# Kernel optimization log

Hardware: AMD Instinct MI355X
Metric: run time of the kernel (lower is better)

## Reference

```python
import jax, jax.numpy as jnp
import numpy as np

N = 50000
E = 800000
IN_DIM = 128
H1 = 512
H2 = 300
OUT_DIM = 10
EPS = 1e-5


def setup_inputs() -> dict:
    key = jax.random.key(0)
    ks = jax.random.split(key, 12)
    x = jax.random.normal(ks[0], (N, IN_DIM), dtype=jnp.float32)
    edge_index = jax.random.randint(ks[1], (2, E), 0, N, dtype=jnp.int64)
    edge_weight = jax.random.uniform(ks[2], (E,), dtype=jnp.float32)
    def glorot(k, fan_in, fan_out):
        lim = np.sqrt(6.0 / (fan_in + fan_out)).astype(np.float32)
        return jax.random.uniform(k, (fan_in, fan_out), jnp.float32, -lim, lim)
    return {
        "x": x,
        "edge_index": edge_index,
        "edge_weight": edge_weight,
        "W1": glorot(ks[3], IN_DIM, H1), "b1": jnp.zeros((H1,), jnp.float32),
        "g1": jnp.ones((H1,), jnp.float32), "beta1": jnp.zeros((H1,), jnp.float32),
        "W2": glorot(ks[4], H1, H2), "b2": jnp.zeros((H2,), jnp.float32),
        "g2": jnp.ones((H2,), jnp.float32), "beta2": jnp.zeros((H2,), jnp.float32),
        "Wl": glorot(ks[5], H2, OUT_DIM), "bl": jnp.zeros((OUT_DIM,), jnp.float32),
    }


def _gcn_norm(edge_index, edge_weight, n):
    # add self loops (fill value 1.0), then symmetric normalization (PyG gcn_norm)
    si = jnp.arange(n, dtype=edge_index.dtype)
    row = jnp.concatenate([edge_index[0], si])  # source
    col = jnp.concatenate([edge_index[1], si])  # target
    w = jnp.concatenate([edge_weight, jnp.ones((n,), edge_weight.dtype)])
    deg = jax.ops.segment_sum(w, col, num_segments=n)
    dis = jnp.where(deg > 0, jax.lax.rsqrt(deg), 0.0)
    return row, col, dis[row] * w * dis[col]


def _propagate(h, row, col, norm, n):
    # gather source rows, weight, scatter-add into targets
    return jax.ops.segment_sum(h[row] * norm[:, None], col, num_segments=n)


def _batchnorm(h, g, beta):
    mean = jnp.mean(h, axis=0)
    var = jnp.mean(jnp.square(h - mean), axis=0)  # biased var (torch BN)
    return (h - mean) * jax.lax.rsqrt(var + EPS) * g + beta


def reference(x, edge_index, edge_weight, W1, b1, g1, beta1,
              W2, b2, g2, beta2, Wl, bl):
    n = x.shape[0]
    row, col, norm = _gcn_norm(edge_index, edge_weight, n)
    # layer 1: aggregate then transform (== GCNConv's lin-then-propagate math)
    h = _propagate(x, row, col, norm, n) @ W1 + b1
    h = jax.nn.relu(_batchnorm(h, g1, beta1))
    # layer 2: transform then aggregate
    h = _propagate(h @ W2, row, col, norm, n) + b2
    h = jax.nn.relu(_batchnorm(h, g2, beta2))
    # classifier head + log_softmax
    h = jax.nn.relu(h @ Wl + bl)
    return jax.nn.log_softmax(h, axis=1)
```

## Files before the change

kernel.cpp:

```cpp
#include <hip/hip_runtime.h>
#include <math.h>

namespace {

constexpr int kIn  = 128;
constexpr int kH1  = 512;
constexpr int kH2  = 300;
constexpr int kH2p = 304;
constexpr int kOut = 10;
constexpr float kEps = 1e-5f;

typedef __attribute__((ext_vector_type(8))) short bf16x8;
typedef __attribute__((ext_vector_type(4))) float f32x4;

__device__ __forceinline__ void atomAddF(float* p, float v) {
  unsafeAtomicAdd(p, v);
}

__device__ __forceinline__ unsigned short f2bf(float f) {
  unsigned u = __builtin_bit_cast(unsigned, f);
  unsigned r = u + 0x7fffu + ((u >> 16) & 1u);
  return (unsigned short)(r >> 16);
}

__device__ __forceinline__ float bf2f(unsigned short h) {
  return __builtin_bit_cast(float, (unsigned)h << 16);
}

__device__ __forceinline__ float blo(unsigned u) {
  return __builtin_bit_cast(float, u << 16);
}
__device__ __forceinline__ float bhi(unsigned u) {
  return __builtin_bit_cast(float, u & 0xffff0000u);
}

__device__ __forceinline__ void fma8(const uint4& q, float w, float* acc) {
  acc[0] = fmaf(blo(q.x), w, acc[0]);
  acc[1] = fmaf(bhi(q.x), w, acc[1]);
  acc[2] = fmaf(blo(q.y), w, acc[2]);
  acc[3] = fmaf(bhi(q.y), w, acc[3]);
  acc[4] = fmaf(blo(q.z), w, acc[4]);
  acc[5] = fmaf(bhi(q.z), w, acc[5]);
  acc[6] = fmaf(blo(q.w), w, acc[6]);
  acc[7] = fmaf(bhi(q.w), w, acc[7]);
}

__global__ void k_init(float* __restrict__ deg, int* __restrict__ cnt, int n) {
  int i = blockIdx.x * blockDim.x + threadIdx.x;
  if (i < n) { deg[i] = 1.0f; cnt[i] = 0; }
}

__global__ void k_deg_cnt(float* __restrict__ deg, int* __restrict__ cnt,
                          const int* __restrict__ ei, const float* __restrict__ w, int nE) {
  int i = blockIdx.x * blockDim.x + threadIdx.x;
  if (i < nE) {
    int c = ei[nE + i];
    atomAddF(&deg[c], w[i]);
    atomicAdd(&cnt[c], 1);
  }
}

__global__ void k_dis(float* __restrict__ deg, int n) {
  int i = blockIdx.x * blockDim.x + threadIdx.x;
  if (i < n) deg[i] = rsqrtf(deg[i]);
}

__global__ __launch_bounds__(1024) void k_scan(int* __restrict__ cnt, int n) {
  __shared__ int wsum[16];
  __shared__ int woff[17];
  const int lane = threadIdx.x & 63;
  const int wid  = threadIdx.x >> 6;
  int carry = 0;
  const int nchunk = (n + 1023) >> 10;
  for (int ch = 0; ch < nchunk; ++ch) {
    int i = (ch << 10) + threadIdx.x;
    int v = (i < n) ? cnt[i] : 0;
    int s = v;
#pragma unroll
    for (int off = 1; off < 64; off <<= 1) {
      int t = __shfl_up(s, off);
      if (lane >= off) s += t;
    }
    if (lane == 63) wsum[wid] = s;
    __syncthreads();
    if (wid == 0 && lane < 16) {
      int u = wsum[lane];
#pragma unroll
      for (int off = 1; off < 16; off <<= 1) {
        int q = __shfl_up(u, off);
        if (lane >= off) u += q;
      }
      woff[lane + 1] = u;
      if (lane == 0) woff[0] = 0;
    }
    __syncthreads();
    int excl = s - v + woff[wid] + carry;
    if (i < n) cnt[i] = excl;
    carry += woff[16];
    __syncthreads();
  }
}

__global__ void k_scatter(int* __restrict__ cnt, const int* __restrict__ ei,
                          const float* __restrict__ w, const float* __restrict__ dis,
                          uint2* __restrict__ pr, int nE) {
  int i = blockIdx.x * blockDim.x + threadIdx.x;
  if (i < nE) {
    int r = ei[i];
    int c = ei[nE + i];
    int pos = atomicAdd(&cnt[c], 1);
    float ww = dis[r] * w[i] * dis[c];
    pr[pos] = make_uint2((unsigned)r, __builtin_bit_cast(unsigned, ww));
  }
}

__global__ void k_xbf(const float* __restrict__ X, unsigned short* __restrict__ O, int total4) {
  int i = blockIdx.x * blockDim.x + threadIdx.x;
  if (i >= total4) return;
  float4 v = reinterpret_cast<const float4*>(X)[i];
  uint2 pk;
  pk.x = (unsigned)f2bf(v.x) | ((unsigned)f2bf(v.y) << 16);
  pk.y = (unsigned)f2bf(v.z) | ((unsigned)f2bf(v.w) << 16);
  reinterpret_cast<uint2*>(O)[i] = pk;
}

__global__ void k_wt(const float* __restrict__ W, unsigned short* __restrict__ WT,
                     int K, int Nsrc, int Npad) {
  int idx = blockIdx.x * blockDim.x + threadIdx.x;
  if (idx >= K * Npad) return;
  int n = idx / K, k = idx - n * K;
  WT[idx] = (n < Nsrc) ? f2bf(W[(size_t)k * Nsrc + n]) : (unsigned short)0;
}

template<int NSQ>
__global__ void k_gather(const unsigned short* __restrict__ X, const int* __restrict__ endp,
                         const uint2* __restrict__ pr, const float* __restrict__ dis,
                         unsigned short* __restrict__ out, int n) {
  int tid = blockIdx.x * blockDim.x + threadIdx.x;
  int v = tid / NSQ;
  int s = tid - v * NSQ;
  if (v >= n) return;
  int beg = (v == 0) ? 0 : endp[v - 1];
  int end = endp[v];
  const uint4* Xr = reinterpret_cast<const uint4*>(X);
  float d = dis[v];
  float sw = d * d;
  float acc[8];
  {
    uint4 q = Xr[(size_t)v * NSQ + s];
    acc[0] = blo(q.x) * sw; acc[1] = bhi(q.x) * sw;
    acc[2] = blo(q.y) * sw; acc[3] = bhi(q.y) * sw;
    acc[4] = blo(q.z) * sw; acc[5] = bhi(q.z) * sw;
    acc[6] = blo(q.w) * sw; acc[7] = bhi(q.w) * sw;
  }
  int e = beg;
  for (; e + 4 <= end; e += 4) {
    uint2 p0 = pr[e], p1 = pr[e + 1], p2 = pr[e + 2], p3 = pr[e + 3];
    uint4 q0 = Xr[(size_t)p0.x * NSQ + s];
    uint4 q1 = Xr[(size_t)p1.x * NSQ + s];
    uint4 q2 = Xr[(size_t)p2.x * NSQ + s];
    uint4 q3 = Xr[(size_t)p3.x * NSQ + s];
    fma8(q0, __builtin_bit_cast(float, p0.y), acc);
    fma8(q1, __builtin_bit_cast(float, p1.y), acc);
    fma8(q2, __builtin_bit_cast(float, p2.y), acc);
    fma8(q3, __builtin_bit_cast(float, p3.y), acc);
  }
  for (; e < end; ++e) {
    uint2 p = pr[e];
    uint4 q = Xr[(size_t)p.x * NSQ + s];
    fma8(q, __builtin_bit_cast(float, p.y), acc);
  }
  uint4 o;
  o.x = (unsigned)f2bf(acc[0]) | ((unsigned)f2bf(acc[1]) << 16);
  o.y = (unsigned)f2bf(acc[2]) | ((unsigned)f2bf(acc[3]) << 16);
  o.z = (unsigned)f2bf(acc[4]) | ((unsigned)f2bf(acc[5]) << 16);
  o.w = (unsigned)f2bf(acc[6]) | ((unsigned)f2bf(acc[7]) << 16);
  reinterpret_cast<uint4*>(out)[(size_t)v * NSQ + s] = o;
}

__global__ __launch_bounds__(256) void k_gemm(const unsigned short* __restrict__ A,
                                              const unsigned short* __restrict__ BT,
                                              unsigned short* __restrict__ C, int M, int Nlog, int K) {
  constexpr int BM = 128, BN = 128, BK = 32;
  __shared__ unsigned short lA[(BK / 8) * BM * 8];
  __shared__ unsigned short lB[(BK / 8) * BN * 8];
  const int tid  = threadIdx.x;
  const int lane = tid & 63;
  const int wid  = tid >> 6;
  const int wr   = wid >> 1;
  const int wc   = wid & 1;
  const int m0 = blockIdx.x * BM;
  const int n0 = blockIdx.y * BN;

  const int sm  = tid >> 2;
  const int sk8 = tid & 3;
  const int fr = lane & 15, fq = lane >> 4;

  f32x4 acc[4][4] = {};

  for (int k0 = 0; k0 < K; k0 += BK) {
    uint4 a0, a1, b0, b1;
    {
      const uint4 z = make_uint4(0, 0, 0, 0);
      int r0 = m0 + sm, r1 = m0 + sm + 64;
      a0 = (r0 < M) ? *reinterpret_cast<const uint4*>(A + (size_t)r0 * K + k0 + sk8 * 8) : z;
      a1 = (r1 < M) ? *reinterpret_cast<const uint4*>(A + (size_t)r1 * K + k0 + sk8 * 8) : z;
      int c0 = n0 + sm, c1 = n0 + sm + 64;
      b0 = (c0 < Nlog) ? *reinterpret_cast<const uint4*>(BT + (size_t)c0 * K + k0 + sk8 * 8) : z;
      b1 = (c1 < Nlog) ? *reinterpret_cast<const uint4*>(BT + (size_t)c1 * K + k0 + sk8 * 8) : z;
    }
    __syncthreads();
    *reinterpret_cast<uint4*>(lA + (sk8 * BM + sm) * 8)      = a0;
    *reinterpret_cast<uint4*>(lA + (sk8 * BM + sm + 64) * 8) = a1;
    *reinterpret_cast<uint4*>(lB + (sk8 * BN + sm) * 8)      = b0;
    *reinterpret_cast<uint4*>(lB + (sk8 * BN + sm + 64) * 8) = b1;
    __syncthreads();

    bf16x8 af[4], bfr[4];
#pragma unroll
    for (int m = 0; m < 4; ++m)
      af[m] = *reinterpret_cast<const bf16x8*>(lA + (fq * BM + wr * 64 + m * 16 + fr) * 8);
#pragma unroll
    for (int nn = 0; nn < 4; ++nn)
      bfr[nn] = *reinterpret_cast<const bf16x8*>(lB + (fq * BN + wc * 64 + nn * 16 + fr) * 8);
#pragma unroll
    for (int m = 0; m < 4; ++m)
#pragma unroll
      for (int nn = 0; nn < 4; ++nn)
        acc[m][nn] = __builtin_amdgcn_mfma_f32_16x16x32_bf16(af[m], bfr[nn], acc[m][nn], 0, 0, 0);
  }

#pragma unroll
  for (int m = 0; m < 4; ++m) {
#pragma unroll
    for (int r = 0; r < 4; ++r) {
      int row = m0 + wr * 64 + m * 16 + fq * 4 + r;
      if (row >= M) continue;
#pragma unroll
      for (int nn = 0; nn < 4; ++nn) {
        int col = n0 + wc * 64 + nn * 16 + fr;
        if (col < Nlog)
          C[(size_t)row * Nlog + col] = f2bf(acc[m][nn][r]);
      }
    }
  }
}

__global__ void k_bn_stats_bf16(const unsigned short* __restrict__ H, float* __restrict__ s1,
                                float* __restrict__ s2, int n, int C, int stride, int rpb) {
  int r0 = blockIdx.x * rpb;
  int r1 = r0 + rpb;
  if (r1 > n) r1 = n;
  for (int c = threadIdx.x; c < C; c += blockDim.x) {
    float a = 0.f, b = 0.f;
    for (int r = r0; r < r1; ++r) {
      float v = bf2f(H[(size_t)r * stride + c]);
      a += v;
      b = fmaf(v, v, b);
    }
    atomAddF(&s1[c], a);
    atomAddF(&s2[c], b);
  }
}

__global__ void k_bn_finalize(const float* __restrict__ s1, const float* __restrict__ s2,
                              const float* __restrict__ g, const float* __restrict__ beta,
                              float* __restrict__ scale, float* __restrict__ shift,
                              int C, float invN) {
  int c = blockIdx.x * blockDim.x + threadIdx.x;
  if (c >= C) return;
  float mean = s1[c] * invN;
  float var = fmaxf(s2[c] * invN - mean * mean, 0.f);
  float sc = g[c] * rsqrtf(var + kEps);
  scale[c] = sc;
  shift[c] = beta[c] - mean * sc;
}

template<int C>
__global__ void k_bn_apply_relu_bf16(unsigned short* __restrict__ H,
                                     const float* __restrict__ scale,
                                     const float* __restrict__ shift, int total8) {
  int i = blockIdx.x * blockDim.x + threadIdx.x;
  if (i >= total8) return;
  uint4 q = reinterpret_cast<uint4*>(H)[i];
  int c = (i * 8) & (C - 1);
  unsigned w[4] = {q.x, q.y, q.z, q.w};
  unsigned o[4];
#pragma unroll
  for (int j = 0; j < 4; ++j) {
    float lo = blo(w[j]);
    float hi = bhi(w[j]);
    int cl = c + j * 2;
    lo = fmaxf(fmaf(lo, scale[cl],     shift[cl]),     0.f);
    hi = fmaxf(fmaf(hi, scale[cl + 1], shift[cl + 1]), 0.f);
    o[j] = (unsigned)f2bf(lo) | ((unsigned)f2bf(hi) << 16);
  }
  reinterpret_cast<uint4*>(H)[i] = make_uint4(o[0], o[1], o[2], o[3]);
}

__global__ __launch_bounds__(256) void k_head(const unsigned short* __restrict__ H,
    const float* __restrict__ scale, const float* __restrict__ shift,
    const float* __restrict__ Wl, const float* __restrict__ bl,
    float* __restrict__ out, int n) {
  __shared__ float sW[kH2 * kOut];
  __shared__ float sScale[kH2], sShift[kH2];
  for (int i = threadIdx.x; i < kH2 * kOut; i += blockDim.x) sW[i] = Wl[i];
  for (int i = threadIdx.x; i < kH2; i += blockDim.x) {
    sScale[i] = scale[i];
    sShift[i] = shift[i];
  }
  __syncthreads();
  float blv[kOut];
#pragma unroll
  for (int j = 0; j < kOut; ++j) blv[j] = bl[j];
  const int lane = threadIdx.x & 63;
  const int wid = (blockIdx.x * blockDim.x + threadIdx.x) >> 6;
  const int nw  = (gridDim.x * blockDim.x) >> 6;
  for (int node = wid; node < n; node += nw) {
    const unsigned short* hrow = H + (size_t)node * kH2p;
    float acc[kOut] = {};
    for (int k = lane; k < kH2; k += 64) {
      float v = fmaxf(fmaf(bf2f(hrow[k]), sScale[k], sShift[k]), 0.f);
      const float* wr = sW + k * kOut;
#pragma unroll
      for (int j = 0; j < kOut; ++j) acc[j] = fmaf(v, wr[j], acc[j]);
    }
#pragma unroll
    for (int j = 0; j < kOut; ++j) {
      float v = acc[j];
      for (int off = 32; off > 0; off >>= 1) v += __shfl_down(v, off);
      acc[j] = v;
    }
    if (lane == 0) {
      float vv[kOut], m = -1e30f;
#pragma unroll
      for (int j = 0; j < kOut; ++j) {
        vv[j] = fmaxf(acc[j] + blv[j], 0.f);
        m = fmaxf(m, vv[j]);
      }
      float s = 0.f;
#pragma unroll
      for (int j = 0; j < kOut; ++j) s += expf(vv[j] - m);
      float lse = m + logf(s);
      float* o = out + (size_t)node * kOut;
#pragma unroll
      for (int j = 0; j < kOut; ++j) o[j] = vv[j] - lse;
    }
  }
}

}

extern "C" void kernel_launch(void* const* d_in, const int* in_sizes, int n_in,
                              void* d_out, int out_size, void* d_ws, size_t ws_size,
                              hipStream_t stream) {
  const float* x   = (const float*)d_in[0];
  const int*   ei  = (const int*)d_in[1];
  const float* ew  = (const float*)d_in[2];
  const float* W1  = (const float*)d_in[3];
  const float* g1  = (const float*)d_in[5];
  const float* be1 = (const float*)d_in[6];
  const float* W2  = (const float*)d_in[7];
  const float* g2  = (const float*)d_in[9];
  const float* be2 = (const float*)d_in[10];
  const float* Wl  = (const float*)d_in[11];
  const float* bl  = (const float*)d_in[12];
  float* out = (float*)d_out;
  float* ws  = (float*)d_ws;

  const int n = in_sizes[0] / kIn;
  const int e = in_sizes[1] / 2;

  float* dis = ws;
  int*   cnt = (int*)(ws + 50048);
  uint2* pr  = (uint2*)(ws + 100096);
  float* st  = ws + 1700096;
  float* s1a = st,        *s2a = st + 512,  *sc1 = st + 1024, *sh1 = st + 1536;
  float* s1b = st + 2048, *s2b = st + 2560, *sc2 = st + 3072, *sh2 = st + 3584;
  unsigned short* xbf = (unsigned short*)(ws + 1704192);
  unsigned short* W1T = (unsigned short*)(ws + 4904192);
  unsigned short* W2T = (unsigned short*)(ws + 4936960);
  unsigned short* slotA = (unsigned short*)(ws + 5014784);
  unsigned short* slotB = (unsigned short*)(ws + 12614784);
  unsigned short* agg1 = slotA;
  unsigned short* t2   = slotA;
  unsigned short* h1   = slotB;
  unsigned short* agg2 = slotB;

  constexpr int TPB = 256;

  k_init<<<(n + TPB - 1) / TPB, TPB, 0, stream>>>(dis, cnt, n);
  k_deg_cnt<<<(e + TPB - 1) / TPB, TPB, 0, stream>>>(dis, cnt, ei, ew, e);
  k_dis<<<(n + TPB - 1) / TPB, TPB, 0, stream>>>(dis, n);
  k_scan<<<1, 1024, 0, stream>>>(cnt, n);
  k_scatter<<<(e + TPB - 1) / TPB, TPB, 0, stream>>>(cnt, ei, ew, dis, pr, e);
  hipMemsetAsync(st, 0, 4096 * sizeof(float), stream);
  k_xbf<<<(n * (kIn / 4) + TPB - 1) / TPB, TPB, 0, stream>>>(x, xbf, n * (kIn / 4));
  k_wt<<<(kIn * kH1 + TPB - 1) / TPB, TPB, 0, stream>>>(W1, W1T, kIn, kH1, kH1);
  k_wt<<<(kH1 * kH2p + TPB - 1) / TPB, TPB, 0, stream>>>(W2, W2T, kH1, kH2, kH2p);

  {
    int tot = n * (kIn / 8);
    k_gather<kIn / 8><<<(tot + TPB - 1) / TPB, TPB, 0, stream>>>(xbf, cnt, pr, dis, agg1, n);
  }
  {
    dim3 g((n + 127) / 128, kH1 / 128);
    k_gemm<<<g, 256, 0, stream>>>(agg1, W1T, h1, n, kH1, kIn);
  }
  k_bn_stats_bf16<<<512, 256, 0, stream>>>(h1, s1a, s2a, n, kH1, kH1, (n + 511) / 512);
  k_bn_finalize<<<(kH1 + 255) / 256, 256, 0, stream>>>(s1a, s2a, g1, be1, sc1, sh1, kH1, 1.0f / n);
  k_bn_apply_relu_bf16<kH1><<<((n * (kH1 / 8)) + TPB - 1) / TPB, TPB, 0, stream>>>(
      h1, sc1, sh1, n * (kH1 / 8));

  {
    dim3 g((n + 127) / 128, (kH2p + 127) / 128);
    k_gemm<<<g, 256, 0, stream>>>(h1, W2T, t2, n, kH2p, kH1);
  }
  {
    int tot = n * (kH2p / 8);
    k_gather<kH2p / 8><<<(tot + TPB - 1) / TPB, TPB, 0, stream>>>(t2, cnt, pr, dis, agg2, n);
  }
  k_bn_stats_bf16<<<512, 256, 0, stream>>>(agg2, s1b, s2b, n, kH2, kH2p, (n + 511) / 512);
  k_bn_finalize<<<(kH2 + 255) / 256, 256, 0, stream>>>(s1b, s2b, g2, be2, sc2, sh2, kH2, 1.0f / n);

  k_head<<<1024, 256, 0, stream>>>(agg2, sc2, sh2, Wl, bl, out, n);
}
```

Baseline: 562.2 us.

## Slice gather features by column for cache locality, fuse BN into GEMM, merge prep kernels

The gather inputs are stored in column-slice-major layout: 8 slices of 16 columns for x, and 8 slices of 40 columns for t2 after padding H2 to 320. Each gather block then works on one slice, so the random row reads touch a smaller working set that fits better in L2. Layer-1 BN+ReLU is applied while loading the A operand of the second GEMM, which drops a separate read-modify-write pass over h1. Conversion, weight transpose and zero-init are merged into a single prep kernel. In exchange the padding adds GEMM and gather work, the edge lists are re-read once per slice, and the workspace needs more separate buffers.

```diff
diff --git a/kernel.cpp b/kernel.cpp
--- a/kernel.cpp
+++ b/kernel.cpp
@@ -6,32 +6,27 @@
 constexpr int kIn  = 128;
 constexpr int kH1  = 512;
 constexpr int kH2  = 300;
-constexpr int kH2p = 304;
+constexpr int kH2p = 320;
 constexpr int kOut = 10;
 constexpr float kEps = 1e-5f;
 
 typedef __attribute__((ext_vector_type(8))) short bf16x8;
 typedef __attribute__((ext_vector_type(4))) float f32x4;
 
-__device__ __forceinline__ void atomAddF(float* p, float v) {
-  unsafeAtomicAdd(p, v);
-}
+__device__ __forceinline__ void atomAddF(float* p, float v) { unsafeAtomicAdd(p, v); }
 
 __device__ __forceinline__ unsigned short f2bf(float f) {
   unsigned u = __builtin_bit_cast(unsigned, f);
   unsigned r = u + 0x7fffu + ((u >> 16) & 1u);
   return (unsigned short)(r >> 16);
 }
-
 __device__ __forceinline__ float bf2f(unsigned short h) {
   return __builtin_bit_cast(float, (unsigned)h << 16);
 }
-
-__device__ __forceinline__ float blo(unsigned u) {
-  return __builtin_bit_cast(float, u << 16);
-}
-__device__ __forceinline__ float bhi(unsigned u) {
-  return __builtin_bit_cast(float, u & 0xffff0000u);
+__device__ __forceinline__ float blo(unsigned u) { return __builtin_bit_cast(float, u << 16); }
+__device__ __forceinline__ float bhi(unsigned u) { return __builtin_bit_cast(float, u & 0xffff0000u); }
+__device__ __forceinline__ unsigned pk2(float a, float b) {
+  return (unsigned)f2bf(a) | ((unsigned)f2bf(b) << 16);
 }
 
 __device__ __forceinline__ void fma8(const uint4& q, float w, float* acc) {
@@ -45,9 +40,41 @@
   acc[7] = fmaf(bhi(q.w), w, acc[7]);
 }
 
-__global__ void k_init(float* __restrict__ deg, int* __restrict__ cnt, int n) {
+__device__ __forceinline__ uint4 bnpack(uint4 q, float4 s0, float4 s1, float4 h0, float4 h1) {
+  uint4 r;
+  r.x = pk2(fmaxf(fmaf(blo(q.x), s0.x, h0.x), 0.f), fmaxf(fmaf(bhi(q.x), s0.y, h0.y), 0.f));
+  r.y = pk2(fmaxf(fmaf(blo(q.y), s0.z, h0.z), 0.f), fmaxf(fmaf(bhi(q.y), s0.w, h0.w), 0.f));
+  r.z = pk2(fmaxf(fmaf(blo(q.z), s1.x, h1.x), 0.f), fmaxf(fmaf(bhi(q.z), s1.y, h1.y), 0.f));
+  r.w = pk2(fmaxf(fmaf(blo(q.w), s1.z, h1.z), 0.f), fmaxf(fmaf(bhi(q.w), s1.w, h1.w), 0.f));
+  return r;
+}
+
+__global__ void k_prep(float* __restrict__ deg, int* __restrict__ cnt,
+                       const float* __restrict__ x, unsigned short* __restrict__ xbf,
+                       float* __restrict__ st,
+                       const float* __restrict__ W1, unsigned short* __restrict__ W1T,
+                       const float* __restrict__ W2, unsigned short* __restrict__ W2T, int n) {
   int i = blockIdx.x * blockDim.x + threadIdx.x;
   if (i < n) { deg[i] = 1.0f; cnt[i] = 0; }
+  if (i < 4096) st[i] = 0.f;
+  if (i < kIn * kH1) {
+    int nn = i / kIn, k = i - nn * kIn;
+    W1T[i] = f2bf(W1[(size_t)k * kH1 + nn]);
+  }
+  if (i < kH2p * kH1) {
+    int nn = i / kH1, k = i - nn * kH1;
+    W2T[i] = (nn < kH2) ? f2bf(W2[(size_t)k * kH2 + nn]) : (unsigned short)0;
+  }
+  if (i < n * 16) {
+    int node = i >> 4, g = i & 15;
+    const float4* xp = reinterpret_cast<const float4*>(x + (size_t)node * kIn + g * 8);
+    float4 v0 = xp[0], v1 = xp[1];
+    uint4 o;
+    o.x = pk2(v0.x, v0.y); o.y = pk2(v0.z, v0.w);
+    o.z = pk2(v1.x, v1.y); o.w = pk2(v1.z, v1.w);
+    int slice = g >> 1, win = g & 1;
+    reinterpret_cast<uint4*>(xbf)[((size_t)slice * n + node) * 2 + win] = o;
+  }
 }
 
 __global__ void k_deg_cnt(float* __restrict__ deg, int* __restrict__ cnt,
@@ -114,35 +141,18 @@
   }
 }
 
-__global__ void k_xbf(const float* __restrict__ X, unsigned short* __restrict__ O, int total4) {
-  int i = blockIdx.x * blockDim.x + threadIdx.x;
-  if (i >= total4) return;
-  float4 v = reinterpret_cast<const float4*>(X)[i];
-  uint2 pk;
-  pk.x = (unsigned)f2bf(v.x) | ((unsigned)f2bf(v.y) << 16);
-  pk.y = (unsigned)f2bf(v.z) | ((unsigned)f2bf(v.w) << 16);
-  reinterpret_cast<uint2*>(O)[i] = pk;
-}
-
-__global__ void k_wt(const float* __restrict__ W, unsigned short* __restrict__ WT,
-                     int K, int Nsrc, int Npad) {
-  int idx = blockIdx.x * blockDim.x + threadIdx.x;
-  if (idx >= K * Npad) return;
-  int n = idx / K, k = idx - n * K;
-  WT[idx] = (n < Nsrc) ? f2bf(W[(size_t)k * Nsrc + n]) : (unsigned short)0;
-}
-
 template<int NSQ>
 __global__ void k_gather(const unsigned short* __restrict__ X, const int* __restrict__ endp,
                          const uint2* __restrict__ pr, const float* __restrict__ dis,
-                         unsigned short* __restrict__ out, int n) {
-  int tid = blockIdx.x * blockDim.x + threadIdx.x;
+                         unsigned short* __restrict__ out, int n, int outStride) {
+  const int slice = blockIdx.x & 7;
+  const int tid = (blockIdx.x >> 3) * blockDim.x + threadIdx.x;
   int v = tid / NSQ;
   int s = tid - v * NSQ;
   if (v >= n) return;
+  const uint4* Xr = reinterpret_cast<const uint4*>(X) + (size_t)slice * n * NSQ;
   int beg = (v == 0) ? 0 : endp[v - 1];
   int end = endp[v];
-  const uint4* Xr = reinterpret_cast<const uint4*>(X);
   float d = dis[v];
   float sw = d * d;
   float acc[8];
@@ -171,16 +181,18 @@
     fma8(q, __builtin_bit_cast(float, p.y), acc);
   }
   uint4 o;
-  o.x = (unsigned)f2bf(acc[0]) | ((unsigned)f2bf(acc[1]) << 16);
-  o.y = (unsigned)f2bf(acc[2]) | ((unsigned)f2bf(acc[3]) << 16);
-  o.z = (unsigned)f2bf(acc[4]) | ((unsigned)f2bf(acc[5]) << 16);
-  o.w = (unsigned)f2bf(acc[6]) | ((unsigned)f2bf(acc[7]) << 16);
-  reinterpret_cast<uint4*>(out)[(size_t)v * NSQ + s] = o;
-}
-
+  o.x = pk2(acc[0], acc[1]);
+  o.y = pk2(acc[2], acc[3]);
+  o.z = pk2(acc[4], acc[5]);
+  o.w = pk2(acc[6], acc[7]);
+  *reinterpret_cast<uint4*>(out + (size_t)v * outStride + slice * (NSQ * 8) + s * 8) = o;
+}
+
+template<bool FUSE_BN, bool SLICED_OUT>
 __global__ __launch_bounds__(256) void k_gemm(const unsigned short* __restrict__ A,
-                                              const unsigned short* __restrict__ BT,
-                                              unsigned short* __restrict__ C, int M, int Nlog, int K) {
+    const unsigned short* __restrict__ BT, unsigned short* __restrict__ C,
+    const float* __restrict__ sc, const float* __restrict__ sh,
+    int M, int Nlog, int K) {
   constexpr int BM = 128, BN = 128, BK = 32;
   __shared__ unsigned short lA[(BK / 8) * BM * 8];
   __shared__ unsigned short lB[(BK / 8) * BN * 8];
@@ -196,18 +208,28 @@
   const int sk8 = tid & 3;
   const int fr = lane & 15, fq = lane >> 4;
 
+  const int r0 = m0 + sm, r1 = m0 + sm + 64;
+  const bool ok0 = r0 < M, ok1 = r1 < M;
+  const int c0r = n0 + sm, c1r = n0 + sm + 64;
+  const bool okb0 = c0r < Nlog, okb1 = c1r < Nlog;
+
   f32x4 acc[4][4] = {};
 
   for (int k0 = 0; k0 < K; k0 += BK) {
     uint4 a0, a1, b0, b1;
-    {
-      const uint4 z = make_uint4(0, 0, 0, 0);
-      int r0 = m0 + sm, r1 = m0 + sm + 64;
-      a0 = (r0 < M) ? *reinterpret_cast<const uint4*>(A + (size_t)r0 * K + k0 + sk8 * 8) : z;
-      a1 = (r1 < M) ? *reinterpret_cast<const uint4*>(A + (size_t)r1 * K + k0 + sk8 * 8) : z;
-      int c0 = n0 + sm, c1 = n0 + sm + 64;
-      b0 = (c0 < Nlog) ? *reinterpret_cast<const uint4*>(BT + (size_t)c0 * K + k0 + sk8 * 8) : z;
-      b1 = (c1 < Nlog) ? *reinterpret_cast<const uint4*>(BT + (size_t)c1 * K + k0 + sk8 * 8) : z;
+    const uint4 z = make_uint4(0, 0, 0, 0);
+    const int kk0 = k0 + sk8 * 8;
+    a0 = ok0 ? *reinterpret_cast<const uint4*>(A + (size_t)r0 * K + kk0) : z;
+    a1 = ok1 ? *reinterpret_cast<const uint4*>(A + (size_t)r1 * K + kk0) : z;
+    b0 = okb0 ? *reinterpret_cast<const uint4*>(BT + (size_t)c0r * K + kk0) : z;
+    b1 = okb1 ? *reinterpret_cast<const uint4*>(BT + (size_t)c1r * K + kk0) : z;
+    if constexpr (FUSE_BN) {
+      float4 s0 = *reinterpret_cast<const float4*>(sc + kk0);
+      float4 s1 = *reinterpret_cast<const float4*>(sc + kk0 + 4);
+      float4 h0 = *reinterpret_cast<const float4*>(sh + kk0);
+      float4 h1 = *reinterpret_cast<const float4*>(sh + kk0 + 4);
+      if (ok0) a0 = bnpack(a0, s0, s1, h0, h1);
+      if (ok1) a1 = bnpack(a1, s0, s1, h0, h1);
     }
     __syncthreads();
     *reinterpret_cast<uint4*>(lA + (sk8 * BM + sm) * 8)      = a0;
@@ -239,8 +261,15 @@
 #pragma unroll
       for (int nn = 0; nn < 4; ++nn) {
         int col = n0 + wc * 64 + nn * 16 + fr;
-        if (col < Nlog)
-          C[(size_t)row * Nlog + col] = f2bf(acc[m][nn][r]);
+        if (col < Nlog) {
+          unsigned short v = f2bf(acc[m][nn][r]);
+          if constexpr (SLICED_OUT) {
+            int slice = col / 40, cw = col - slice * 40;
+            C[((size_t)slice * M + row) * 40 + cw] = v;
+          } else {
+            C[(size_t)row * Nlog + col] = v;
+          }
+        }
       }
     }
   }
@@ -274,28 +303,6 @@
   float sc = g[c] * rsqrtf(var + kEps);
   scale[c] = sc;
   shift[c] = beta[c] - mean * sc;
-}
-
-template<int C>
-__global__ void k_bn_apply_relu_bf16(unsigned short* __restrict__ H,
-                                     const float* __restrict__ scale,
-                                     const float* __restrict__ shift, int total8) {
-  int i = blockIdx.x * blockDim.x + threadIdx.x;
-  if (i >= total8) return;
-  uint4 q = reinterpret_cast<uint4*>(H)[i];
-  int c = (i * 8) & (C - 1);
-  unsigned w[4] = {q.x, q.y, q.z, q.w};
-  unsigned o[4];
-#pragma unroll
-  for (int j = 0; j < 4; ++j) {
-    float lo = blo(w[j]);
-    float hi = bhi(w[j]);
-    int cl = c + j * 2;
-    lo = fmaxf(fmaf(lo, scale[cl],     shift[cl]),     0.f);
-    hi = fmaxf(fmaf(hi, scale[cl + 1], shift[cl + 1]), 0.f);
-    o[j] = (unsigned)f2bf(lo) | ((unsigned)f2bf(hi) << 16);
-  }
-  reinterpret_cast<uint4*>(H)[i] = make_uint4(o[0], o[1], o[2], o[3]);
 }
 
 __global__ __launch_bounds__(256) void k_head(const unsigned short* __restrict__ H,
@@ -380,45 +387,37 @@
   unsigned short* xbf = (unsigned short*)(ws + 1704192);
   unsigned short* W1T = (unsigned short*)(ws + 4904192);
   unsigned short* W2T = (unsigned short*)(ws + 4936960);
-  unsigned short* slotA = (unsigned short*)(ws + 5014784);
-  unsigned short* slotB = (unsigned short*)(ws + 12614784);
-  unsigned short* agg1 = slotA;
-  unsigned short* t2   = slotA;
-  unsigned short* h1   = slotB;
-  unsigned short* agg2 = slotB;
+  unsigned short* agg1 = (unsigned short*)(ws + 5018880);
+  unsigned short* h1   = (unsigned short*)(ws + 8218880);
+  unsigned short* t2   = (unsigned short*)(ws + 21018880);
+  unsigned short* agg2 = (unsigned short*)(ws + 29018880);
 
   constexpr int TPB = 256;
 
-  k_init<<<(n + TPB - 1) / TPB, TPB, 0, stream>>>(dis, cnt, n);
+  k_prep<<<(n * 16 + TPB - 1) / TPB, TPB, 0, stream>>>(dis, cnt, x, xbf, st, W1, W1T, W2, W2T, n);
   k_deg_cnt<<<(e + TPB - 1) / TPB, TPB, 0, stream>>>(dis, cnt, ei, ew, e);
   k_dis<<<(n + TPB - 1) / TPB, TPB, 0, stream>>>(dis, n);
   k_scan<<<1, 1024, 0, stream>>>(cnt, n);
   k_scatter<<<(e + TPB - 1) / TPB, TPB, 0, stream>>>(cnt, ei, ew, dis, pr, e);
-  hipMemsetAsync(st, 0, 4096 * sizeof(float), stream);
-  k_xbf<<<(n * (kIn / 4) + TPB - 1) / TPB, TPB, 0, stream>>>(x, xbf, n * (kIn / 4));
-  k_wt<<<(kIn * kH1 + TPB - 1) / TPB, TPB, 0, stream>>>(W1, W1T, kIn, kH1, kH1);
-  k_wt<<<(kH1 * kH2p + TPB - 1) / TPB, TPB, 0, stream>>>(W2, W2T, kH1, kH2, kH2p);
 
   {
-    int tot = n * (kIn / 8);
-    k_gather<kIn / 8><<<(tot + TPB - 1) / TPB, TPB, 0, stream>>>(xbf, cnt, pr, dis, agg1, n);
+    int bps = (n * 2 + TPB - 1) / TPB;
+    k_gather<2><<<bps * 8, TPB, 0, stream>>>(xbf, cnt, pr, dis, agg1, n, kIn);
   }
   {
     dim3 g((n + 127) / 128, kH1 / 128);
-    k_gemm<<<g, 256, 0, stream>>>(agg1, W1T, h1, n, kH1, kIn);
+    k_gemm<false, false><<<g, 256, 0, stream>>>(agg1, W1T, h1, nullptr, nullptr, n, kH1, kIn);
   }
   k_bn_stats_bf16<<<512, 256, 0, stream>>>(h1, s1a, s2a, n, kH1, kH1, (n + 511) / 512);
   k_bn_finalize<<<(kH1 + 255) / 256, 256, 0, stream>>>(s1a, s2a, g1, be1, sc1, sh1, kH1, 1.0f / n);
-  k_bn_apply_relu_bf16<kH1><<<((n * (kH1 / 8)) + TPB - 1) / TPB, TPB, 0, stream>>>(
-      h1, sc1, sh1, n * (kH1 / 8));
 
   {
     dim3 g((n + 127) / 128, (kH2p + 127) / 128);
-    k_gemm<<<g, 256, 0, stream>>>(h1, W2T, t2, n, kH2p, kH1);
+    k_gemm<true, true><<<g, 256, 0, stream>>>(h1, W2T, t2, sc1, sh1, n, kH2p, kH1);
   }
   {
-    int tot = n * (kH2p / 8);
-    k_gather<kH2p / 8><<<(tot + TPB - 1) / TPB, TPB, 0, stream>>>(t2, cnt, pr, dis, agg2, n);
+    int bps = (n * 5 + TPB - 1) / TPB;
+    k_gather<5><<<bps * 8, TPB, 0, stream>>>(t2, cnt, pr, dis, agg2, n, kH2p);
   }
   k_bn_stats_bf16<<<512, 256, 0, stream>>>(agg2, s1b, s2b, n, kH2, kH2p, (n + 511) / 512);
   k_bn_finalize<<<(kH2 + 255) / 256, 256, 0, stream>>>(s1b, s2b, g2, be2, sc2, sh2, kH2, 1.0f / n);
```

Result: slower. 634.5 us (+12.9%).
